# Performance work log

Measured on AMD Instinct MI355X. Metric: run time of the kernel, lower is better.

The kernel has to match this reference:

```python
import jax, jax.numpy as jnp
import numpy as np

N, M, D_IN, D_OUT = 4096, 16384, 256, 256


def setup_inputs() -> dict:
    key = jax.random.key(0)
    k1, k2, k3, k4 = jax.random.split(key, 4)
    query = jax.random.normal(k1, (N, D_IN), dtype=jnp.float32)
    # bandwidths bounded away from zero for numerical sanity
    std = jax.random.uniform(k2, (N,), dtype=jnp.float32, minval=0.5, maxval=1.5)
    source_db = jax.random.normal(k3, (M, D_OUT), dtype=jnp.float32)
    target_db = jax.random.normal(k4, (M, D_IN), dtype=jnp.float32)
    return {"query": query, "std": std, "source_db": source_db, "target_db": target_db}


def reference(query, std, source_db, target_db):
    # Squared L2 distances [N, M] via the GEMM expansion (avoids the NxMxD diff
    # tensor the torch code materializes; same math).
    q_sq = jnp.sum(query * query, axis=1, keepdims=True)          # [N, 1]
    t_sq = jnp.sum(target_db * target_db, axis=1)                 # [M]
    cross = query @ target_db.T                                   # [N, M]
    dist = q_sq + t_sq[None, :] - 2.0 * cross                     # [N, M]
    # Gaussian kernel logits and stable softmax over the database axis.
    x = -dist / (2.0 * std[:, None] ** 2)                         # [N, M]
    w = jax.nn.softmax(x, axis=1)                                 # [N, M]
    # Nadaraya-Watson weighted sum of source values -> [N, D_OUT].
    return w @ source_db
```

## Files before the change

kernel.cpp:

```cpp
#include <hip/hip_runtime.h>


#define N_Q 4096
#define M_DB 16384
#define D_K 256
#define NCC 17
#define BQ 256
#define BM 32
#define NCHUNK 16
#define MC (M_DB / NCHUNK)
#define NTILE (MC / BM)
#define LOG2E 1.44269504088896f
#define THR 8.0f
#define TOFF 17408
#define TILE_B 33792

typedef _Float16 f16;
typedef _Float16 f16x2v __attribute__((ext_vector_type(2)));
typedef _Float16 f16x4v __attribute__((ext_vector_type(4)));
typedef _Float16 f16x8 __attribute__((ext_vector_type(8)));
typedef float f32x16 __attribute__((ext_vector_type(16)));
typedef unsigned short u16;
typedef unsigned int u32;
typedef u32 u32x4 __attribute__((ext_vector_type(4)));

typedef const __attribute__((address_space(1))) void cg_void;
typedef __attribute__((address_space(3))) void lds_void;

__device__ __forceinline__ void gload16(const void* g, void* s) {
  __builtin_amdgcn_global_load_lds((cg_void*)g, (lds_void*)s, 16, 0, 0);
}

__global__ void k_prep_q(const float* __restrict__ q, char* __restrict__ qpk) {
  int qt = blockIdx.x;
  int t = threadIdx.x;
  for (int i = 0; i < 5; i++) {
    int slot = t + 256 * i;
    if (slot >= NCC * 64) break;
    int c = slot >> 6, l = slot & 63;
    int row = qt * 32 + (l & 31);
    int k0 = c * 16 + (l >> 5) * 8;
    f16x8 o;
    for (int e = 0; e < 8; e++) {
      int k = k0 + e;
      float v = (k < D_K) ? q[(size_t)row * D_K + k] : ((k <= D_K + 1) ? 1.0f : 0.0f);
      o[e] = (f16)v;
    }
    *(f16x8*)(qpk + (size_t)qt * TOFF + slot * 16) = o;
  }
}

__global__ void k_prep_t(const float* __restrict__ tdb, char* __restrict__ pkTV) {
  int ti = blockIdx.x;
  int t = threadIdx.x;
  __shared__ float tsq[32];
  {
    int r = t >> 3, seg = t & 7;
    const float* p = tdb + (size_t)(ti * 32 + r) * D_K + seg * 32;
    float s = 0.f;
    for (int j = 0; j < 32; j++) { float x = p[j]; s += x * x; }
    s += __shfl_xor(s, 1); s += __shfl_xor(s, 2); s += __shfl_xor(s, 4);
    if (seg == 0) tsq[r] = 0.5f * s;
  }
  __syncthreads();
  for (int i = 0; i < 5; i++) {
    int slot = t + 256 * i;
    if (slot >= NCC * 64) break;
    int c = slot >> 6, l = slot & 63;
    int row = l & 31;
    int k0 = c * 16 + (l >> 5) * 8;
    float ts = tsq[row];
    f16 th = (f16)(-ts);
    f16x8 o;
    for (int e = 0; e < 8; e++) {
      int k = k0 + e;
      f16 h;
      if (k < D_K)            h = (f16)tdb[(size_t)(ti * 32 + row) * D_K + k];
      else if (k == D_K)      h = th;
      else if (k == D_K + 1)  h = (f16)(-ts - (float)th);
      else                    h = (f16)0.f;
      o[e] = h;
    }
    *(f16x8*)(pkTV + (size_t)ti * TILE_B + slot * 16) = o;
  }
}

__global__ void k_prep_v(const float* __restrict__ src, char* __restrict__ pkTV) {
  int ti = blockIdx.x;
  int t = threadIdx.x;
  for (int i = 0; i < 4; i++) {
    int slot = t + 256 * i;
    int sub = slot >> 6, l = slot & 63;
    int kh = sub >> 3, db = sub & 7;
    int m = ti * 32 + kh * 16 + (l >> 5) * 8;
    int d = db * 32 + (l & 31);
    f16x8 o;
    for (int e = 0; e < 8; e++) o[e] = (f16)src[(size_t)(m + e) * D_K + d];
    *(f16x8*)(pkTV + (size_t)ti * TILE_B + TOFF + slot * 16) = o;
  }
}

__launch_bounds__(512, 2)
__global__ void k_main(const char* __restrict__ qpk, const char* __restrict__ pkTV,
                       const float* __restrict__ stdv,
                       u16* __restrict__ pO, float* __restrict__ pm, float* __restrict__ pl)
{
  __shared__ __align__(16) char su[4 * TILE_B];

  const int bid = blockIdx.x, chunk = bid & 15, qblk = bid >> 4;
  const int tid = threadIdx.x;
  const int w = tid >> 6, l = tid & 63;
  const int lq = l & 31, hi = l >> 5;

  const int qrow = qblk * BQ + w * 32 + lq;
  const float sd = stdv[qrow];
  const float is2l = LOG2E / (sd * sd);

  f16x8 qf[NCC];
  {
    const char* qb = qpk + (size_t)(qblk * 8 + w) * TOFF + l * 16;
#pragma unroll
    for (int c = 0; c < NCC; c++) qf[c] = *(const f16x8*)(qb + c * 1024);
  }

  f32x16 acc[8];
#pragma unroll
  for (int db = 0; db < 8; db++)
#pragma unroll
    for (int j = 0; j < 16; j++) acc[db][j] = 0.f;
  float mrun = -3.0e38f, lrun = 0.f;

  const size_t tbase = (size_t)chunk * NTILE;

  auto stage = [&](int t, int buf) {
    const char* g = pkTV + (tbase + t) * TILE_B;
    char* sb = &su[0] + buf * TILE_B;
#pragma unroll
    for (int i = 0; i < 4; i++)
      gload16(g + i * 8192 + tid * 16, sb + i * 8192 + w * 1024);
    if (l < 8) gload16(g + 32768 + w * 128 + l * 16, sb + 32768 + w * 128);
  };

  stage(0, 0); stage(1, 1); stage(2, 2);
  asm volatile("s_waitcnt vmcnt(10)" ::: "memory");
  __builtin_amdgcn_s_barrier();

  for (int t = 0; t < NTILE; ++t) {
    const int cur = t & 3;
    if (t + 3 < NTILE) stage(t + 3, (t + 3) & 3);

    f32x16 sA, sB;
#pragma unroll
    for (int j = 0; j < 16; j++) { sA[j] = 0.f; sB[j] = 0.f; }
    const char* tb = &su[0] + cur * TILE_B + l * 16;
    __builtin_amdgcn_s_setprio(1);
#pragma unroll
    for (int c = 0; c < NCC - 1; c += 2) {
      sA = __builtin_amdgcn_mfma_f32_32x32x16_f16(*(const f16x8*)(tb + c * 1024), qf[c], sA, 0, 0, 0);
      sB = __builtin_amdgcn_mfma_f32_32x32x16_f16(*(const f16x8*)(tb + (c + 1) * 1024), qf[c + 1], sB, 0, 0, 0);
    }
    sA = __builtin_amdgcn_mfma_f32_32x32x16_f16(*(const f16x8*)(tb + 16 * 1024), qf[16], sA, 0, 0, 0);
    __builtin_amdgcn_s_setprio(0);

    float l2[16];
#pragma unroll
    for (int j = 0; j < 16; j++) l2[j] = (sA[j] + sB[j]) * is2l;

    float a0 = fmaxf(l2[0], l2[1]),  a1 = fmaxf(l2[2], l2[3]);
    float a2 = fmaxf(l2[4], l2[5]),  a3 = fmaxf(l2[6], l2[7]);
    float a4 = fmaxf(l2[8], l2[9]),  a5 = fmaxf(l2[10], l2[11]);
    float a6 = fmaxf(l2[12], l2[13]), a7 = fmaxf(l2[14], l2[15]);
    float px = fmaxf(fmaxf(fmaxf(a0, a1), fmaxf(a2, a3)),
                     fmaxf(fmaxf(a4, a5), fmaxf(a6, a7)));
    px = fmaxf(px, __shfl_xor(px, 32));

    if (__any(px > mrun + THR)) {
      const float mnew = fmaxf(mrun, px);
      const float cl = exp2f(mrun - mnew);
      mrun = mnew; lrun *= cl;
#pragma unroll
      for (int db = 0; db < 8; db++)
#pragma unroll
        for (int j = 0; j < 16; j++) acc[db][j] *= cl;
    }
    float pr[16];
#pragma unroll
    for (int j = 0; j < 16; j++) pr[j] = exp2f(l2[j] - mrun);
    float s0 = (pr[0] + pr[1]) + (pr[2] + pr[3]);
    float s1 = (pr[4] + pr[5]) + (pr[6] + pr[7]);
    float s2 = (pr[8] + pr[9]) + (pr[10] + pr[11]);
    float s3 = (pr[12] + pr[13]) + (pr[14] + pr[15]);
    float ls = (s0 + s1) + (s2 + s3);
    ls += __shfl_xor(ls, 32);
    lrun += ls;

    u32 pk[8], xk[8];
#pragma unroll
    for (int j = 0; j < 8; j++) {
      f16x2v v; v[0] = (f16)pr[2 * j]; v[1] = (f16)pr[2 * j + 1];
      pk[j] = __builtin_bit_cast(u32, v);
    }
#pragma unroll
    for (int j = 0; j < 8; j++) xk[j] = (u32)__shfl_xor((int)pk[j], 32);
    const bool h = (hi != 0);
    u32x4 w0 = { h ? xk[2] : pk[0], h ? xk[3] : pk[1],
                 h ? pk[2] : xk[0], h ? pk[3] : xk[1] };
    u32x4 w1 = { h ? xk[6] : pk[4], h ? xk[7] : pk[5],
                 h ? pk[6] : xk[4], h ? pk[7] : xk[5] };
    f16x8 B0 = __builtin_bit_cast(f16x8, w0);
    f16x8 B1 = __builtin_bit_cast(f16x8, w1);

    const char* vb = &su[0] + cur * TILE_B + TOFF + l * 16;
    __builtin_amdgcn_s_setprio(1);
#pragma unroll
    for (int db = 0; db < 8; db++)
      acc[db] = __builtin_amdgcn_mfma_f32_32x32x16_f16(*(const f16x8*)(vb + db * 1024), B0, acc[db], 0, 0, 0);
#pragma unroll
    for (int db = 0; db < 8; db++)
      acc[db] = __builtin_amdgcn_mfma_f32_32x32x16_f16(*(const f16x8*)(vb + 8192 + db * 1024), B1, acc[db], 0, 0, 0);
    __builtin_amdgcn_s_setprio(0);

    if (t < NTILE - 1) {
      if (t < NTILE - 3)       asm volatile("s_waitcnt vmcnt(10)" ::: "memory");
      else if (t == NTILE - 3) asm volatile("s_waitcnt vmcnt(5)" ::: "memory");
      else                     asm volatile("s_waitcnt vmcnt(0)" ::: "memory");
      __builtin_amdgcn_s_barrier();
    }
  }

  const float inv = 1.0f / lrun;
#pragma unroll
  for (int db = 0; db < 8; db++) {
#pragma unroll
    for (int g = 0; g < 4; g++) {
      f16x4v o4;
#pragma unroll
      for (int r4 = 0; r4 < 4; r4++) o4[r4] = (f16)(acc[db][g * 4 + r4] * inv);
      const int d = db * 32 + g * 8 + hi * 4;
      *(f16x4v*)(pO + ((size_t)chunk * N_Q + qrow) * D_K + d) = o4;
    }
  }
  if (hi == 0) {
    pm[(size_t)chunk * N_Q + qrow] = mrun;
    pl[(size_t)chunk * N_Q + qrow] = lrun;
  }
}

__global__ void k_combine(const u16* __restrict__ pO, const float* __restrict__ pm,
                          const float* __restrict__ pl, float* __restrict__ out)
{
  int n = blockIdx.x, d = threadIdx.x;
  float M = -3.0e38f;
#pragma unroll
  for (int c = 0; c < NCHUNK; c++) M = fmaxf(M, pm[(size_t)c * N_Q + n]);
  float den = 0.f, num = 0.f;
#pragma unroll
  for (int c = 0; c < NCHUNK; c++) {
    float wl = exp2f(pm[(size_t)c * N_Q + n] - M) * pl[(size_t)c * N_Q + n];
    den += wl;
    float v = (float)(*(const f16*)(pO + ((size_t)c * N_Q + n) * D_K + d));
    num += wl * v;
  }
  out[(size_t)n * D_K + d] = num / den;
}

extern "C" void kernel_launch(void* const* d_in, const int* in_sizes, int n_in,
                              void* d_out, int out_size, void* d_ws, size_t ws_size,
                              hipStream_t stream)
{
  const float* q    = (const float*)d_in[0];
  const float* stdv = (const float*)d_in[1];
  const float* src  = (const float*)d_in[2];
  const float* tdb  = (const float*)d_in[3];
  float* out = (float*)d_out;

  char* wsp = (char*)d_ws;
  char* qpk = wsp;        wsp += (size_t)(N_Q / 32) * TOFF;
  char* pkTV = wsp;       wsp += (size_t)(M_DB / 32) * TILE_B;
  u16* pO = (u16*)wsp;    wsp += (size_t)NCHUNK * N_Q * D_K * 2;
  float* pm = (float*)wsp; wsp += (size_t)NCHUNK * N_Q * 4;
  float* pl = (float*)wsp; wsp += (size_t)NCHUNK * N_Q * 4;

  hipLaunchKernelGGL(k_prep_q, dim3(N_Q / 32), dim3(256), 0, stream, q, qpk);
  hipLaunchKernelGGL(k_prep_t, dim3(M_DB / 32), dim3(256), 0, stream, tdb, pkTV);
  hipLaunchKernelGGL(k_prep_v, dim3(M_DB / 32), dim3(256), 0, stream, src, pkTV);
  hipLaunchKernelGGL(k_main,   dim3((N_Q / BQ) * NCHUNK), dim3(512), 0, stream,
                     qpk, pkTV, stdv, pO, pm, pl);
  hipLaunchKernelGGL(k_combine, dim3(N_Q), dim3(256), 0, stream, pO, pm, pl, out);
}
```

Measured before the change: 122.6 us.

## Pair tiles per barrier, fuse T/V prep kernels, vectorize combine

The main loop now stages two tiles at a time into the 4-slot LDS ring and processes two tiles between barriers, with a full vmcnt(0) wait per pair. This halves the barrier count but gives a shallower, burstier prefetch. The target and value packing kernels are merged into one launch, and the combine kernel now handles 8 rows per block with 8-wide f16 loads and vector f32 stores, cutting launch count and memory transactions.

```diff
diff --git a/kernel.cpp b/kernel.cpp
--- a/kernel.cpp
+++ b/kernel.cpp
@@ -19,6 +19,7 @@
 typedef _Float16 f16x2v __attribute__((ext_vector_type(2)));
 typedef _Float16 f16x4v __attribute__((ext_vector_type(4)));
 typedef _Float16 f16x8 __attribute__((ext_vector_type(8)));
+typedef float f32x4 __attribute__((ext_vector_type(4)));
 typedef float f32x16 __attribute__((ext_vector_type(16)));
 typedef unsigned short u16;
 typedef unsigned int u32;
@@ -50,7 +51,8 @@
   }
 }
 
-__global__ void k_prep_t(const float* __restrict__ tdb, char* __restrict__ pkTV) {
+__global__ void k_prep_tv(const float* __restrict__ tdb, const float* __restrict__ src,
+                          char* __restrict__ pkTV) {
   int ti = blockIdx.x;
   int t = threadIdx.x;
   __shared__ float tsq[32];
@@ -83,11 +85,6 @@
     }
     *(f16x8*)(pkTV + (size_t)ti * TILE_B + slot * 16) = o;
   }
-}
-
-__global__ void k_prep_v(const float* __restrict__ src, char* __restrict__ pkTV) {
-  int ti = blockIdx.x;
-  int t = threadIdx.x;
   for (int i = 0; i < 4; i++) {
     int slot = t + 256 * i;
     int sub = slot >> 6, l = slot & 63;
@@ -141,14 +138,8 @@
     if (l < 8) gload16(g + 32768 + w * 128 + l * 16, sb + 32768 + w * 128);
   };
 
-  stage(0, 0); stage(1, 1); stage(2, 2);
-  asm volatile("s_waitcnt vmcnt(10)" ::: "memory");
-  __builtin_amdgcn_s_barrier();
-
-  for (int t = 0; t < NTILE; ++t) {
+  auto body = [&](int t) {
     const int cur = t & 3;
-    if (t + 3 < NTILE) stage(t + 3, (t + 3) & 3);
-
     f32x16 sA, sB;
 #pragma unroll
     for (int j = 0; j < 16; j++) { sA[j] = 0.f; sB[j] = 0.f; }
@@ -219,11 +210,20 @@
     for (int db = 0; db < 8; db++)
       acc[db] = __builtin_amdgcn_mfma_f32_32x32x16_f16(*(const f16x8*)(vb + 8192 + db * 1024), B1, acc[db], 0, 0, 0);
     __builtin_amdgcn_s_setprio(0);
-
-    if (t < NTILE - 1) {
-      if (t < NTILE - 3)       asm volatile("s_waitcnt vmcnt(10)" ::: "memory");
-      else if (t == NTILE - 3) asm volatile("s_waitcnt vmcnt(5)" ::: "memory");
-      else                     asm volatile("s_waitcnt vmcnt(0)" ::: "memory");
+  };
+
+  stage(0, 0);
+  stage(1, 1);
+  asm volatile("s_waitcnt vmcnt(0)" ::: "memory");
+  __builtin_amdgcn_s_barrier();
+
+  for (int s = 0; s < NTILE; s += 2) {
+    if (s + 2 < NTILE) stage(s + 2, (s + 2) & 3);
+    if (s + 3 < NTILE) stage(s + 3, (s + 3) & 3);
+    body(s);
+    body(s + 1);
+    if (s + 2 < NTILE) {
+      asm volatile("s_waitcnt vmcnt(0)" ::: "memory");
       __builtin_amdgcn_s_barrier();
     }
   }
@@ -249,19 +249,31 @@
 __global__ void k_combine(const u16* __restrict__ pO, const float* __restrict__ pm,
                           const float* __restrict__ pl, float* __restrict__ out)
 {
-  int n = blockIdx.x, d = threadIdx.x;
+  const int t = threadIdx.x;
+  const int n = blockIdx.x * 8 + (t >> 5);
+  const int j = t & 31;
   float M = -3.0e38f;
 #pragma unroll
   for (int c = 0; c < NCHUNK; c++) M = fmaxf(M, pm[(size_t)c * N_Q + n]);
-  float den = 0.f, num = 0.f;
+  float den = 0.f;
+  float o[8];
+#pragma unroll
+  for (int e = 0; e < 8; e++) o[e] = 0.f;
 #pragma unroll
   for (int c = 0; c < NCHUNK; c++) {
-    float wl = exp2f(pm[(size_t)c * N_Q + n] - M) * pl[(size_t)c * N_Q + n];
+    const float wl = exp2f(pm[(size_t)c * N_Q + n] - M) * pl[(size_t)c * N_Q + n];
     den += wl;
-    float v = (float)(*(const f16*)(pO + ((size_t)c * N_Q + n) * D_K + d));
-    num += wl * v;
-  }
-  out[(size_t)n * D_K + d] = num / den;
+    const f16x8 v = *(const f16x8*)(pO + ((size_t)c * N_Q + n) * D_K + j * 8);
+#pragma unroll
+    for (int e = 0; e < 8; e++) o[e] += wl * (float)v[e];
+  }
+  const float inv = 1.0f / den;
+  f32x4 w0, w1;
+#pragma unroll
+  for (int e = 0; e < 4; e++) { w0[e] = o[e] * inv; w1[e] = o[4 + e] * inv; }
+  float* dst = out + (size_t)n * D_K + j * 8;
+  *(f32x4*)dst = w0;
+  *(f32x4*)(dst + 4) = w1;
 }
 
 extern "C" void kernel_launch(void* const* d_in, const int* in_sizes, int n_in,
@@ -281,10 +293,9 @@
   float* pm = (float*)wsp; wsp += (size_t)NCHUNK * N_Q * 4;
   float* pl = (float*)wsp; wsp += (size_t)NCHUNK * N_Q * 4;
 
-  hipLaunchKernelGGL(k_prep_q, dim3(N_Q / 32), dim3(256), 0, stream, q, qpk);
-  hipLaunchKernelGGL(k_prep_t, dim3(M_DB / 32), dim3(256), 0, stream, tdb, pkTV);
-  hipLaunchKernelGGL(k_prep_v, dim3(M_DB / 32), dim3(256), 0, stream, src, pkTV);
-  hipLaunchKernelGGL(k_main,   dim3((N_Q / BQ) * NCHUNK), dim3(512), 0, stream,
+  hipLaunchKernelGGL(k_prep_q,  dim3(N_Q / 32), dim3(256), 0, stream, q, qpk);
+  hipLaunchKernelGGL(k_prep_tv, dim3(M_DB / 32), dim3(256), 0, stream, tdb, src, pkTV);
+  hipLaunchKernelGGL(k_main,    dim3((N_Q / BQ) * NCHUNK), dim3(512), 0, stream,
                      qpk, pkTV, stdv, pO, pm, pl);
-  hipLaunchKernelGGL(k_combine, dim3(N_Q), dim3(256), 0, stream, pO, pm, pl, out);
-}
+  hipLaunchKernelGGL(k_combine, dim3(N_Q / 8), dim3(256), 0, stream, pO, pm, pl, out);
+}
```

Result: faster. 117.2 us (-4.4%).
